# Kernel optimization log

Hardware: AMD Instinct MI355X
Metric: run time of the kernel (lower is better)

Reference implementation:

```python
import jax, jax.numpy as jnp
import numpy as np

N_NODES = 100000
N_EDGES = 500000
HIDDEN = 32
HEADS = 4
PROJ = HIDDEN * HEADS  # 128
LN_EPS = 1e-5


def setup_inputs() -> dict:
    key = jax.random.key(0)
    ks = jax.random.split(key, 12)
    # Xavier-uniform bound for Linear(3, PROJ): sqrt(6/(3+PROJ))
    b_qkv = float(np.sqrt(6.0 / (3 + PROJ)))
    b_out = float(np.sqrt(6.0 / (PROJ + HIDDEN)))
    return {
        "positions": jax.random.normal(ks[0], (N_NODES, 3), dtype=jnp.float32),
        "edge_index": jax.random.randint(ks[1], (2, N_EDGES), 0, N_NODES, dtype=jnp.int64),
        "Wq": jax.random.uniform(ks[2], (3, PROJ), jnp.float32, -b_qkv, b_qkv),
        "bq": jnp.zeros((PROJ,), jnp.float32),
        "Wk": jax.random.uniform(ks[3], (3, PROJ), jnp.float32, -b_qkv, b_qkv),
        "bk": jnp.zeros((PROJ,), jnp.float32),
        "Wv": jax.random.uniform(ks[4], (3, PROJ), jnp.float32, -b_qkv, b_qkv),
        "bv": jnp.zeros((PROJ,), jnp.float32),
        "Wout": jax.random.uniform(ks[5], (PROJ, HIDDEN), jnp.float32, -b_out, b_out),
        "bout": jnp.zeros((HIDDEN,), jnp.float32),
        "gamma": jnp.ones((HIDDEN,), jnp.float32),
        "beta": jnp.zeros((HIDDEN,), jnp.float32),
    }


def reference(positions, edge_index, Wq, bq, Wk, bk, Wv, bv, Wout, bout, gamma, beta):
    row, col = edge_index[0], edge_index[1]
    rel = positions[row] - positions[col]                      # [E, 3]
    E = rel.shape[0]
    q = (rel @ Wq + bq).reshape(E, HEADS, HIDDEN)              # [E, H, D]
    k = (rel @ Wk + bk).reshape(E, HEADS, HIDDEN)
    v = (rel @ Wv + bv).reshape(E, HEADS, HIDDEN)
    # attention score per (edge, head), softmax over heads
    scores = jnp.sum(q * k, axis=-1) / jnp.sqrt(jnp.float32(HIDDEN))  # [E, H]
    attn = jax.nn.softmax(scores, axis=-1)                     # dropout is identity in eval
    wv = (attn[..., None] * v).reshape(E, PROJ)                # [E, H*D]
    # scatter-mean over destination nodes (col), dim_size = N
    seg_sum = jax.ops.segment_sum(wv, col, num_segments=N_NODES)
    counts = jax.ops.segment_sum(jnp.ones((E,), wv.dtype), col, num_segments=N_NODES)
    mean = seg_sum / jnp.maximum(counts, 1.0)[:, None]         # [N, H*D]
    out = mean @ Wout + bout                                   # [N, D]
    mu = jnp.mean(out, axis=-1, keepdims=True)
    var = jnp.var(out, axis=-1, keepdims=True)
    out = (out - mu) / jnp.sqrt(var + LN_EPS) * gamma + beta
    return jax.nn.silu(out)
```

## Files before the change

### kernel.cpp

```cpp
#include <hip/hip_runtime.h>
#include <hip/hip_fp16.h>

#define LN_EPS 1e-5f
#define NREP 4

typedef _Float16 f16x2 __attribute__((ext_vector_type(2)));
typedef _Float16 f16x8 __attribute__((ext_vector_type(8)));

__device__ __forceinline__ void pk_atomic_add_u32(_Float16* p, unsigned bits) {
  f16x2 v = __builtin_bit_cast(f16x2, bits);
#if __has_builtin(__builtin_amdgcn_flat_atomic_fadd_v2f16)
  __builtin_amdgcn_flat_atomic_fadd_v2f16((f16x2*)p, v);
#else
  unsafeAtomicAdd((__half2*)p, *(__half2*)&v);
#endif
}

__device__ __forceinline__ unsigned pack2(float a, float b) {
  f16x2 v;
  v.x = (_Float16)a;
  v.y = (_Float16)b;
  return __builtin_bit_cast(unsigned, v);
}


__global__ __launch_bounds__(256) void precompute_kernel(
    const float* __restrict__ Wq, const float* __restrict__ bq,
    const float* __restrict__ Wk, const float* __restrict__ bk,
    const float* __restrict__ Wv, const float* __restrict__ bv,
    const float* __restrict__ Wout, float* __restrict__ coef,
    float* __restrict__ T, uint4* __restrict__ zbase, int zcount) {
  __shared__ float sW[1024];
  __shared__ float sM[4][3][32];
  __shared__ float sCv[4][32];
  const int t = threadIdx.x;
  const float scale = 0.17677669529663687f;

  if (blockIdx.x == 0) {
    for (int i = t; i < 384; i += 256) {
      sW[i] = Wq[i];
      sW[384 + i] = Wk[i];
    }
    if (t < 128) {
      sW[768 + t] = bq[t];
      sW[896 + t] = bk[t];
    }
    __syncthreads();

    if (t < 40) {
      const int h = t / 10, j = t % 10;
      float acc = 0.f;
#pragma unroll 4
      for (int d = 0; d < 32; ++d) {
        const int idx = h * 32 + d;
        float q0 = sW[idx], q1 = sW[128 + idx], q2 = sW[256 + idx];
        float k0 = sW[384 + idx], k1 = sW[512 + idx], k2 = sW[640 + idx];
        float bqv = sW[768 + idx], bkv = sW[896 + idx];
        float v;
        switch (j) {
          case 0: v = q0 * k0; break;
          case 1: v = q1 * k1; break;
          case 2: v = q2 * k2; break;
          case 3: v = q0 * k1 + q1 * k0; break;
          case 4: v = q0 * k2 + q2 * k0; break;
          case 5: v = q1 * k2 + q2 * k1; break;
          case 6: v = q0 * bkv + k0 * bqv; break;
          case 7: v = q1 * bkv + k1 * bqv; break;
          case 8: v = q2 * bkv + k2 * bqv; break;
          default: v = bqv * bkv; break;
        }
        acc += v;
      }
      coef[t] = acc * scale;
    }
  } else if (blockIdx.x == 1) {
    if (t < 128) {
      const int h = t >> 5, o = t & 31;
      float m0 = 0, m1 = 0, m2 = 0, cv = 0;
      for (int d = 0; d < 32; ++d) {
        const int j = h * 32 + d;
        const float w = Wout[j * 32 + o];
        m0 += Wv[j] * w;
        m1 += Wv[128 + j] * w;
        m2 += Wv[256 + j] * w;
        cv += bv[j] * w;
      }
      sM[h][0][o] = m0;
      sM[h][1][o] = m1;
      sM[h][2][o] = m2;
      sCv[h][o] = cv;
    }
    __syncthreads();

    if (t < 128) {
      for (int idx = t; idx < 512; idx += 128) {
        const int j = idx >> 5, col = idx & 31;
        float v;
        if (j < 3)        v = sCv[j][col] - sCv[3][col];
        else if (j < 6)   v = sM[3][j - 3][col];
        else if (j < 15)  { const int h2 = (j - 6) / 3, i = (j - 6) % 3; v = sM[h2][i][col] - sM[3][i][col]; }
        else              v = sCv[3][col];
        T[idx] = v;
      }
    }
  } else {
    const uint4 z = {0u, 0u, 0u, 0u};
    const int stride = (gridDim.x - 2) * 256;
    for (int i = (blockIdx.x - 2) * 256 + t; i < zcount; i += stride)
      zbase[i] = z;
  }
}

__global__ __launch_bounds__(256) void edge_kernel(
    const float* __restrict__ pos, const int* __restrict__ ei, int E,
    const float* __restrict__ coef, _Float16* __restrict__ fsums, int N) {
  __shared__ unsigned sF[8][264];
  __shared__ int sC[256];

  const int t = threadIdx.x;
  const int lane64 = t & 63;

  bool pz = true;
  if (lane64 < 8) pz = (ei[2 * lane64 + 1] == 0);
  const unsigned long long bz = __ballot(pz);
  const int i64 = (int)__builtin_amdgcn_readfirstlane(bz == ~0ull ? 1 : 0);

  const int base = blockIdx.x * 256;
  const int vb = min(256, E - base);
  const int e = base + t;

  int c = 0;
  float px0 = 0, px1 = 0, px2 = 0, pc0 = 0, pc1 = 0, pc2 = 0;
  if (t < vb) {
    int r;
    if (i64) {
      r = ((const int2*)ei)[(size_t)e].x;
      c = ((const int2*)ei)[(size_t)E + (size_t)e].x;
    } else {
      r = ei[e];
      c = ei[(size_t)E + e];
    }
    px0 = pos[r * 3 + 0]; px1 = pos[r * 3 + 1]; px2 = pos[r * 3 + 2];
    pc0 = pos[c * 3 + 0]; pc1 = pos[c * 3 + 1]; pc2 = pos[c * 3 + 2];
  }

  if (t < vb) {
    const float rx = px0 - pc0;
    const float ry = px1 - pc1;
    const float rz = px2 - pc2;
    float s[4];
#pragma unroll
    for (int h = 0; h < 4; ++h) {
      const float* cf = coef + h * 10;
      s[h] = cf[9] + rx * cf[6] + ry * cf[7] + rz * cf[8] + rx * rx * cf[0] +
             ry * ry * cf[1] + rz * rz * cf[2] + rx * ry * cf[3] +
             rx * rz * cf[4] + ry * rz * cf[5];
    }
    const float mx = fmaxf(fmaxf(s[0], s[1]), fmaxf(s[2], s[3]));
    const float e0 = __expf(s[0] - mx), e1 = __expf(s[1] - mx);
    const float e2 = __expf(s[2] - mx), e3 = __expf(s[3] - mx);
    const float inv = 1.0f / (e0 + e1 + e2 + e3);
    const float a0 = e0 * inv, a1 = e1 * inv, a2 = e2 * inv;

    sC[t] = c;
    sF[0][t] = pack2(a0, a1);
    sF[1][t] = pack2(a2, rx);
    sF[2][t] = pack2(ry, rz);
    sF[3][t] = pack2(a0 * rx, a0 * ry);
    sF[4][t] = pack2(a0 * rz, a1 * rx);
    sF[5][t] = pack2(a1 * ry, a1 * rz);
    sF[6][t] = pack2(a2 * rx, a2 * ry);
    sF[7][t] = pack2(a2 * rz, 1.0f);
  }
  __syncthreads();

  _Float16* fr = fsums + (size_t)(blockIdx.x & (NREP - 1)) * ((size_t)N * 16);
  const int w = t >> 6;
  const int slot = lane64 & 7;
  const int esub = lane64 >> 3;
#pragma unroll
  for (int i = 0; i < 8; ++i) {
    const int g = w * 64 + i * 8 + esub;
    if (g < vb) {
      const int ct = sC[g];
      const unsigned val = sF[slot][g];
      pk_atomic_add_u32(fr + (size_t)ct * 16 + 2 * slot, val);
    }
  }
}

__global__ __launch_bounds__(256) void node_kernel(
    const _Float16* __restrict__ fsums, const float* __restrict__ T,
    const float* __restrict__ bout, const float* __restrict__ gamma,
    const float* __restrict__ beta, float* __restrict__ out, int N) {
  const int tid = blockIdx.x * blockDim.x + threadIdx.x;
  const int node = tid >> 5;
  const int col = tid & 31;
  if (node >= N) return;

  float f[16];
#pragma unroll
  for (int j = 0; j < 16; ++j) f[j] = 0.f;
  const size_t rstride = (size_t)N * 16;
#pragma unroll
  for (int r = 0; r < NREP; ++r) {
    const f16x8* fp = (const f16x8*)(fsums + r * rstride + (size_t)node * 16);
    const f16x8 va = fp[0];
    const f16x8 vb = fp[1];
#pragma unroll
    for (int j = 0; j < 8; ++j) {
      f[j] += (float)va[j];
      f[8 + j] += (float)vb[j];
    }
  }
  const float invc = 1.0f / fmaxf(f[15], 1.0f);

  float acc = 0.f;
#pragma unroll
  for (int j = 0; j < 16; ++j) acc = fmaf(f[j], T[j * 32 + col], acc);
  acc = fmaf(acc, invc, bout[col]);

  float sx = acc, sx2 = acc * acc;
#pragma unroll
  for (int off = 16; off >= 1; off >>= 1) {
    sx += __shfl_xor(sx, off);
    sx2 += __shfl_xor(sx2, off);
  }
  const float mu = sx * (1.0f / 32.0f);
  const float var = sx2 * (1.0f / 32.0f) - mu * mu;
  const float inv = rsqrtf(var + LN_EPS);
  const float y = (acc - mu) * inv * gamma[col] + beta[col];
  const float o = y * (1.0f / (1.0f + __expf(-y)));
  out[(size_t)node * 32 + col] = o;
}

extern "C" void kernel_launch(void* const* d_in, const int* in_sizes, int n_in,
                              void* d_out, int out_size, void* d_ws, size_t ws_size,
                              hipStream_t stream) {
  const float* pos  = (const float*)d_in[0];
  const int*   ei   = (const int*)d_in[1];
  const float* Wq   = (const float*)d_in[2];
  const float* bq   = (const float*)d_in[3];
  const float* Wk   = (const float*)d_in[4];
  const float* bk   = (const float*)d_in[5];
  const float* Wv   = (const float*)d_in[6];
  const float* bv   = (const float*)d_in[7];
  const float* Wout = (const float*)d_in[8];
  const float* bout = (const float*)d_in[9];
  const float* gam  = (const float*)d_in[10];
  const float* bet  = (const float*)d_in[11];

  const int N = in_sizes[0] / 3;
  const int E = in_sizes[1] / 2;

  _Float16* fsums = (_Float16*)d_ws;
  float* coef = (float*)((char*)d_ws + (size_t)NREP * N * 32);
  float* T = coef + 48;

  const int zcount = (int)(((size_t)NREP * N * 32) / 16);
  precompute_kernel<<<256, 256, 0, stream>>>(Wq, bq, Wk, bk, Wv, bv, Wout,
                                             coef, T, (uint4*)d_ws, zcount);

  const int edge_blocks = (E + 255) / 256;
  edge_kernel<<<edge_blocks, 256, 0, stream>>>(pos, ei, E, coef, fsums, N);

  const int node_blocks = (int)(((size_t)N * 32 + 255) / 256);
  node_kernel<<<node_blocks, 256, 0, stream>>>(fsums, T, bout, gam, bet,
                                               (float*)d_out, N);

  (void)n_in; (void)out_size; (void)ws_size;
}
```

Baseline: 145.8 us.

## Fuse edge scatter and node epilogue into one persistent kernel with grid barrier

Merges the edge scatter-add kernel and the node normalisation kernel into one persistent kernel. Blocks loop over edge chunks, then meet at a software grid barrier (atomic counter plus spin-sleep) before a grid-stride pass over nodes. It also drops the four replicated fp16 accumulation buffers in favour of a single buffer, which cuts zeroing and reduction traffic but raises atomic contention. The spin barrier needs all blocks to be co-resident; the grid is capped at 1024 blocks with launch bounds of 4 blocks per CU to make that hold.

New measurement: 342.0 us. 2.34x slower.

```diff
diff --git a/kernel.cpp b/kernel.cpp
--- a/kernel.cpp
+++ b/kernel.cpp
@@ -2,7 +2,6 @@
 #include <hip/hip_fp16.h>
 
 #define LN_EPS 1e-5f
-#define NREP 4
 
 typedef _Float16 f16x2 __attribute__((ext_vector_type(2)));
 typedef _Float16 f16x8 __attribute__((ext_vector_type(8)));
@@ -29,7 +28,8 @@
     const float* __restrict__ Wk, const float* __restrict__ bk,
     const float* __restrict__ Wv, const float* __restrict__ bv,
     const float* __restrict__ Wout, float* __restrict__ coef,
-    float* __restrict__ T, uint4* __restrict__ zbase, int zcount) {
+    float* __restrict__ T, unsigned* __restrict__ ctr,
+    uint4* __restrict__ zbase, int zcount) {
   __shared__ float sW[1024];
   __shared__ float sM[4][3][32];
   __shared__ float sCv[4][32];
@@ -104,6 +104,7 @@
       }
     }
   } else {
+    if (blockIdx.x == 2 && t == 0) *ctr = 0u;
     const uint4 z = {0u, 0u, 0u, 0u};
     const int stride = (gridDim.x - 2) * 256;
     for (int i = (blockIdx.x - 2) * 256 + t; i < zcount; i += stride)
@@ -111,9 +112,12 @@
   }
 }
 
-__global__ __launch_bounds__(256) void edge_kernel(
-    const float* __restrict__ pos, const int* __restrict__ ei, int E,
-    const float* __restrict__ coef, _Float16* __restrict__ fsums, int N) {
+__global__ __launch_bounds__(256, 4) void fused_kernel(
+    const float* __restrict__ pos, const int* __restrict__ ei, int E, int N,
+    const float* __restrict__ coef, const float* __restrict__ T,
+    const float* __restrict__ bout, const float* __restrict__ gamma,
+    const float* __restrict__ beta, _Float16* __restrict__ fsums,
+    unsigned* __restrict__ ctr, float* __restrict__ out, int nchunks) {
   __shared__ unsigned sF[8][264];
   __shared__ int sC[256];
 
@@ -125,113 +129,111 @@
   const unsigned long long bz = __ballot(pz);
   const int i64 = (int)__builtin_amdgcn_readfirstlane(bz == ~0ull ? 1 : 0);
 
-  const int base = blockIdx.x * 256;
-  const int vb = min(256, E - base);
-  const int e = base + t;
-
-  int c = 0;
-  float px0 = 0, px1 = 0, px2 = 0, pc0 = 0, pc1 = 0, pc2 = 0;
-  if (t < vb) {
-    int r;
-    if (i64) {
-      r = ((const int2*)ei)[(size_t)e].x;
-      c = ((const int2*)ei)[(size_t)E + (size_t)e].x;
-    } else {
-      r = ei[e];
-      c = ei[(size_t)E + e];
-    }
-    px0 = pos[r * 3 + 0]; px1 = pos[r * 3 + 1]; px2 = pos[r * 3 + 2];
-    pc0 = pos[c * 3 + 0]; pc1 = pos[c * 3 + 1]; pc2 = pos[c * 3 + 2];
-  }
-
-  if (t < vb) {
-    const float rx = px0 - pc0;
-    const float ry = px1 - pc1;
-    const float rz = px2 - pc2;
-    float s[4];
-#pragma unroll
-    for (int h = 0; h < 4; ++h) {
-      const float* cf = coef + h * 10;
-      s[h] = cf[9] + rx * cf[6] + ry * cf[7] + rz * cf[8] + rx * rx * cf[0] +
-             ry * ry * cf[1] + rz * rz * cf[2] + rx * ry * cf[3] +
-             rx * rz * cf[4] + ry * rz * cf[5];
-    }
-    const float mx = fmaxf(fmaxf(s[0], s[1]), fmaxf(s[2], s[3]));
-    const float e0 = __expf(s[0] - mx), e1 = __expf(s[1] - mx);
-    const float e2 = __expf(s[2] - mx), e3 = __expf(s[3] - mx);
-    const float inv = 1.0f / (e0 + e1 + e2 + e3);
-    const float a0 = e0 * inv, a1 = e1 * inv, a2 = e2 * inv;
-
-    sC[t] = c;
-    sF[0][t] = pack2(a0, a1);
-    sF[1][t] = pack2(a2, rx);
-    sF[2][t] = pack2(ry, rz);
-    sF[3][t] = pack2(a0 * rx, a0 * ry);
-    sF[4][t] = pack2(a0 * rz, a1 * rx);
-    sF[5][t] = pack2(a1 * ry, a1 * rz);
-    sF[6][t] = pack2(a2 * rx, a2 * ry);
-    sF[7][t] = pack2(a2 * rz, 1.0f);
-  }
-  __syncthreads();
-
-  _Float16* fr = fsums + (size_t)(blockIdx.x & (NREP - 1)) * ((size_t)N * 16);
   const int w = t >> 6;
   const int slot = lane64 & 7;
   const int esub = lane64 >> 3;
-#pragma unroll
-  for (int i = 0; i < 8; ++i) {
-    const int g = w * 64 + i * 8 + esub;
-    if (g < vb) {
-      const int ct = sC[g];
-      const unsigned val = sF[slot][g];
-      pk_atomic_add_u32(fr + (size_t)ct * 16 + 2 * slot, val);
-    }
-  }
-}
-
-__global__ __launch_bounds__(256) void node_kernel(
-    const _Float16* __restrict__ fsums, const float* __restrict__ T,
-    const float* __restrict__ bout, const float* __restrict__ gamma,
-    const float* __restrict__ beta, float* __restrict__ out, int N) {
-  const int tid = blockIdx.x * blockDim.x + threadIdx.x;
-  const int node = tid >> 5;
-  const int col = tid & 31;
-  if (node >= N) return;
-
-  float f[16];
-#pragma unroll
-  for (int j = 0; j < 16; ++j) f[j] = 0.f;
-  const size_t rstride = (size_t)N * 16;
-#pragma unroll
-  for (int r = 0; r < NREP; ++r) {
-    const f16x8* fp = (const f16x8*)(fsums + r * rstride + (size_t)node * 16);
+
+  for (int cb = blockIdx.x; cb < nchunks; cb += gridDim.x) {
+    const int base = cb * 256;
+    const int vb = min(256, E - base);
+    const int e = base + t;
+
+    if (t < vb) {
+      int r, c;
+      if (i64) {
+        r = ((const int2*)ei)[(size_t)e].x;
+        c = ((const int2*)ei)[(size_t)E + (size_t)e].x;
+      } else {
+        r = ei[e];
+        c = ei[(size_t)E + e];
+      }
+      const float rx = pos[r * 3 + 0] - pos[c * 3 + 0];
+      const float ry = pos[r * 3 + 1] - pos[c * 3 + 1];
+      const float rz = pos[r * 3 + 2] - pos[c * 3 + 2];
+      float s[4];
+#pragma unroll
+      for (int h = 0; h < 4; ++h) {
+        const float* cf = coef + h * 10;
+        s[h] = cf[9] + rx * cf[6] + ry * cf[7] + rz * cf[8] + rx * rx * cf[0] +
+               ry * ry * cf[1] + rz * rz * cf[2] + rx * ry * cf[3] +
+               rx * rz * cf[4] + ry * rz * cf[5];
+      }
+      const float mx = fmaxf(fmaxf(s[0], s[1]), fmaxf(s[2], s[3]));
+      const float e0 = __expf(s[0] - mx), e1 = __expf(s[1] - mx);
+      const float e2 = __expf(s[2] - mx), e3 = __expf(s[3] - mx);
+      const float inv = 1.0f / (e0 + e1 + e2 + e3);
+      const float a0 = e0 * inv, a1 = e1 * inv, a2 = e2 * inv;
+
+      sC[t] = c;
+      sF[0][t] = pack2(a0, a1);
+      sF[1][t] = pack2(a2, rx);
+      sF[2][t] = pack2(ry, rz);
+      sF[3][t] = pack2(a0 * rx, a0 * ry);
+      sF[4][t] = pack2(a0 * rz, a1 * rx);
+      sF[5][t] = pack2(a1 * ry, a1 * rz);
+      sF[6][t] = pack2(a2 * rx, a2 * ry);
+      sF[7][t] = pack2(a2 * rz, 1.0f);
+    }
+    __syncthreads();
+
+#pragma unroll
+    for (int i = 0; i < 8; ++i) {
+      const int g = w * 64 + i * 8 + esub;
+      if (g < vb) {
+        const int ct = sC[g];
+        const unsigned val = sF[slot][g];
+        pk_atomic_add_u32(fsums + (size_t)ct * 16 + 2 * slot, val);
+      }
+    }
+    __syncthreads();
+  }
+
+  __threadfence();
+  if (t == 0) {
+    atomicAdd(ctr, 1u);
+    while (atomicAdd(ctr, 0u) < (unsigned)gridDim.x)
+      __builtin_amdgcn_s_sleep(8);
+  }
+  __syncthreads();
+  __threadfence();
+
+  const int col = t & 31;
+  float tc[16];
+#pragma unroll
+  for (int j = 0; j < 16; ++j) tc[j] = T[j * 32 + col];
+  const float bo = bout[col], ga = gamma[col], be = beta[col];
+
+  const int groups = gridDim.x * 8;
+  for (int node = blockIdx.x * 8 + (t >> 5); node < N; node += groups) {
+    const f16x8* fp = (const f16x8*)(fsums + (size_t)node * 16);
     const f16x8 va = fp[0];
     const f16x8 vb = fp[1];
+    float f[16];
 #pragma unroll
     for (int j = 0; j < 8; ++j) {
-      f[j] += (float)va[j];
-      f[8 + j] += (float)vb[j];
-    }
-  }
-  const float invc = 1.0f / fmaxf(f[15], 1.0f);
-
-  float acc = 0.f;
-#pragma unroll
-  for (int j = 0; j < 16; ++j) acc = fmaf(f[j], T[j * 32 + col], acc);
-  acc = fmaf(acc, invc, bout[col]);
-
-  float sx = acc, sx2 = acc * acc;
-#pragma unroll
-  for (int off = 16; off >= 1; off >>= 1) {
-    sx += __shfl_xor(sx, off);
-    sx2 += __shfl_xor(sx2, off);
-  }
-  const float mu = sx * (1.0f / 32.0f);
-  const float var = sx2 * (1.0f / 32.0f) - mu * mu;
-  const float inv = rsqrtf(var + LN_EPS);
-  const float y = (acc - mu) * inv * gamma[col] + beta[col];
-  const float o = y * (1.0f / (1.0f + __expf(-y)));
-  out[(size_t)node * 32 + col] = o;
+      f[j] = (float)va[j];
+      f[8 + j] = (float)vb[j];
+    }
+    const float invc = 1.0f / fmaxf(f[15], 1.0f);
+
+    float acc = 0.f;
+#pragma unroll
+    for (int j = 0; j < 16; ++j) acc = fmaf(f[j], tc[j], acc);
+    acc = fmaf(acc, invc, bo);
+
+    float sx = acc, sx2 = acc * acc;
+#pragma unroll
+    for (int off = 16; off >= 1; off >>= 1) {
+      sx += __shfl_xor(sx, off);
+      sx2 += __shfl_xor(sx2, off);
+    }
+    const float mu = sx * (1.0f / 32.0f);
+    const float var = sx2 * (1.0f / 32.0f) - mu * mu;
+    const float inv = rsqrtf(var + LN_EPS);
+    const float y = (acc - mu) * inv * ga + be;
+    const float o = y * (1.0f / (1.0f + __expf(-y)));
+    out[(size_t)node * 32 + col] = o;
+  }
 }
 
 extern "C" void kernel_launch(void* const* d_in, const int* in_sizes, int n_in,
@@ -254,19 +256,21 @@
   const int E = in_sizes[1] / 2;
 
   _Float16* fsums = (_Float16*)d_ws;
-  float* coef = (float*)((char*)d_ws + (size_t)NREP * N * 32);
+  float* coef = (float*)((char*)d_ws + (size_t)N * 32);
   float* T = coef + 48;
-
-  const int zcount = (int)(((size_t)NREP * N * 32) / 16);
-  precompute_kernel<<<256, 256, 0, stream>>>(Wq, bq, Wk, bk, Wv, bv, Wout,
-                                             coef, T, (uint4*)d_ws, zcount);
-
-  const int edge_blocks = (E + 255) / 256;
-  edge_kernel<<<edge_blocks, 256, 0, stream>>>(pos, ei, E, coef, fsums, N);
-
-  const int node_blocks = (int)(((size_t)N * 32 + 255) / 256);
-  node_kernel<<<node_blocks, 256, 0, stream>>>(fsums, T, bout, gam, bet,
-                                               (float*)d_out, N);
+  unsigned* ctr = (unsigned*)(coef + 560);
+
+  const int zcount = (int)(((size_t)N * 32) / 16);
+  precompute_kernel<<<130, 256, 0, stream>>>(Wq, bq, Wk, bk, Wv, bv, Wout,
+                                             coef, T, ctr, (uint4*)d_ws,
+                                             zcount);
+
+  const int nchunks = (E + 255) / 256;
+  int g = (nchunks + 1) / 2;
+  if (g > 1024) g = 1024;
+  if (g < 1) g = 1;
+  fused_kernel<<<g, 256, 0, stream>>>(pos, ei, E, N, coef, T, bout, gam, bet,
+                                      fsums, ctr, (float*)d_out, nchunks);
 
   (void)n_in; (void)out_size; (void)ws_size;
 }
```

## Drop replicated fp16 accumulators and make node kernel grid-stride

Applied to the files above, without the earlier changes.

Removes the four-way replication of the per-node fp16 atomic accumulation buffers, so edges scatter into a single buffer. Zeroing traffic and node-kernel reads fall by four, and fewer zeroing blocks are launched. The node kernel becomes grid-stride, loading the T, bias and LayerNorm parameters once per thread and reusing them across nodes. The cost is more atomic contention on the shared addresses and more fp16 rounding from accumulating into one copy.

Measured after the change: 133.6 us. -8.4%, faster.

```diff
diff --git a/kernel.cpp b/kernel.cpp
--- a/kernel.cpp
+++ b/kernel.cpp
@@ -2,7 +2,6 @@
 #include <hip/hip_fp16.h>
 
 #define LN_EPS 1e-5f
-#define NREP 4
 
 typedef _Float16 f16x2 __attribute__((ext_vector_type(2)));
 typedef _Float16 f16x8 __attribute__((ext_vector_type(8)));
@@ -113,7 +112,7 @@
 
 __global__ __launch_bounds__(256) void edge_kernel(
     const float* __restrict__ pos, const int* __restrict__ ei, int E,
-    const float* __restrict__ coef, _Float16* __restrict__ fsums, int N) {
+    const float* __restrict__ coef, _Float16* __restrict__ fsums) {
   __shared__ unsigned sF[8][264];
   __shared__ int sC[256];
 
@@ -174,7 +173,6 @@
   }
   __syncthreads();
 
-  _Float16* fr = fsums + (size_t)(blockIdx.x & (NREP - 1)) * ((size_t)N * 16);
   const int w = t >> 6;
   const int slot = lane64 & 7;
   const int esub = lane64 >> 3;
@@ -184,7 +182,7 @@
     if (g < vb) {
       const int ct = sC[g];
       const unsigned val = sF[slot][g];
-      pk_atomic_add_u32(fr + (size_t)ct * 16 + 2 * slot, val);
+      pk_atomic_add_u32(fsums + (size_t)ct * 16 + 2 * slot, val);
     }
   }
 }
@@ -193,45 +191,45 @@
     const _Float16* __restrict__ fsums, const float* __restrict__ T,
     const float* __restrict__ bout, const float* __restrict__ gamma,
     const float* __restrict__ beta, float* __restrict__ out, int N) {
-  const int tid = blockIdx.x * blockDim.x + threadIdx.x;
-  const int node = tid >> 5;
-  const int col = tid & 31;
-  if (node >= N) return;
-
-  float f[16];
-#pragma unroll
-  for (int j = 0; j < 16; ++j) f[j] = 0.f;
-  const size_t rstride = (size_t)N * 16;
-#pragma unroll
-  for (int r = 0; r < NREP; ++r) {
-    const f16x8* fp = (const f16x8*)(fsums + r * rstride + (size_t)node * 16);
+  const int t = threadIdx.x;
+  const int col = t & 31;
+
+  float tc[16];
+#pragma unroll
+  for (int j = 0; j < 16; ++j) tc[j] = T[j * 32 + col];
+  const float bo = bout[col], ga = gamma[col], be = beta[col];
+
+  const int groups = gridDim.x * 8;
+  for (int node = blockIdx.x * 8 + (t >> 5); node < N; node += groups) {
+    const f16x8* fp = (const f16x8*)(fsums + (size_t)node * 16);
     const f16x8 va = fp[0];
     const f16x8 vb = fp[1];
+    float f[16];
 #pragma unroll
     for (int j = 0; j < 8; ++j) {
-      f[j] += (float)va[j];
-      f[8 + j] += (float)vb[j];
-    }
-  }
-  const float invc = 1.0f / fmaxf(f[15], 1.0f);
-
-  float acc = 0.f;
-#pragma unroll
-  for (int j = 0; j < 16; ++j) acc = fmaf(f[j], T[j * 32 + col], acc);
-  acc = fmaf(acc, invc, bout[col]);
-
-  float sx = acc, sx2 = acc * acc;
-#pragma unroll
-  for (int off = 16; off >= 1; off >>= 1) {
-    sx += __shfl_xor(sx, off);
-    sx2 += __shfl_xor(sx2, off);
-  }
-  const float mu = sx * (1.0f / 32.0f);
-  const float var = sx2 * (1.0f / 32.0f) - mu * mu;
-  const float inv = rsqrtf(var + LN_EPS);
-  const float y = (acc - mu) * inv * gamma[col] + beta[col];
-  const float o = y * (1.0f / (1.0f + __expf(-y)));
-  out[(size_t)node * 32 + col] = o;
+      f[j] = (float)va[j];
+      f[8 + j] = (float)vb[j];
+    }
+    const float invc = 1.0f / fmaxf(f[15], 1.0f);
+
+    float acc = 0.f;
+#pragma unroll
+    for (int j = 0; j < 16; ++j) acc = fmaf(f[j], tc[j], acc);
+    acc = fmaf(acc, invc, bo);
+
+    float sx = acc, sx2 = acc * acc;
+#pragma unroll
+    for (int off = 16; off >= 1; off >>= 1) {
+      sx += __shfl_xor(sx, off);
+      sx2 += __shfl_xor(sx2, off);
+    }
+    const float mu = sx * (1.0f / 32.0f);
+    const float var = sx2 * (1.0f / 32.0f) - mu * mu;
+    const float inv = rsqrtf(var + LN_EPS);
+    const float y = (acc - mu) * inv * ga + be;
+    const float o = y * (1.0f / (1.0f + __expf(-y)));
+    out[(size_t)node * 32 + col] = o;
+  }
 }
 
 extern "C" void kernel_launch(void* const* d_in, const int* in_sizes, int n_in,
@@ -254,17 +252,18 @@
   const int E = in_sizes[1] / 2;
 
   _Float16* fsums = (_Float16*)d_ws;
-  float* coef = (float*)((char*)d_ws + (size_t)NREP * N * 32);
+  float* coef = (float*)((char*)d_ws + (size_t)N * 32);
   float* T = coef + 48;
 
-  const int zcount = (int)(((size_t)NREP * N * 32) / 16);
-  precompute_kernel<<<256, 256, 0, stream>>>(Wq, bq, Wk, bk, Wv, bv, Wout,
+  const int zcount = (int)(((size_t)N * 32) / 16);
+  precompute_kernel<<<130, 256, 0, stream>>>(Wq, bq, Wk, bk, Wv, bv, Wout,
                                              coef, T, (uint4*)d_ws, zcount);
 
   const int edge_blocks = (E + 255) / 256;
-  edge_kernel<<<edge_blocks, 256, 0, stream>>>(pos, ei, E, coef, fsums, N);
-
-  const int node_blocks = (int)(((size_t)N * 32 + 255) / 256);
+  edge_kernel<<<edge_blocks, 256, 0, stream>>>(pos, ei, E, coef, fsums);
+
+  int node_blocks = (N + 8 * 10 - 1) / (8 * 10);
+  if (node_blocks > 2048) node_blocks = 2048;
   node_kernel<<<node_blocks, 256, 0, stream>>>(fsums, T, bout, gam, bet,
                                                (float*)d_out, N);
 
```
